# Kernel tuning notes

Measured on AMD Instinct MI355X. Metric: run time of the kernel, lower is better.

## Reference

```python
import jax, jax.numpy as jnp
import numpy as np
import math

# real<->complex packing matching the module's _c2r/_r2c (trailing dim 2)
def _r2c(x):
    return x[..., 0] + 1j * x[..., 1]

H, N, CH, RANK, LMAX = 256, 64, 1, 1, 2048


def setup_inputs() -> dict:
    key = jax.random.key(0)
    k0, k1, k2, k3, k4, k5 = jax.random.split(key, 6)
    C = jax.random.normal(k0, (CH, H, N, 2), jnp.float32)
    B = jax.random.normal(k1, (1, H, N, 2), jnp.float32)
    P = 0.3 * jax.random.normal(k2, (RANK, H, N, 2), jnp.float32)
    # w must have negative real part (Hurwitz) so Cauchy denominators stay away from zero
    w_re = -(jnp.abs(jax.random.normal(k3, (H, N))) * 0.5 + 0.1)
    w_im = jnp.pi * jax.random.normal(k4, (H, N))
    w = jnp.stack([w_re, w_im], axis=-1).astype(jnp.float32)
    log_dt = jax.random.uniform(k5, (H,), jnp.float32,
                                math.log(1e-3), math.log(1e-1))
    return {"C": C, "B": B, "P": P, "w": w, "log_dt": log_dt, "L": LMAX}


def reference(C, B, P, w, log_dt, L):
    Cc = _r2c(C)            # (c, H, N) complex
    Bc = _r2c(B)            # (1, H, N)
    Pc = _r2c(P)            # (r, H, N)
    wc = _r2c(w)            # (H, N)
    Qc = jnp.conj(Pc)       # Q = P.conj() (resolve_conj path)
    dt = jnp.exp(log_dt)    # (H,)

    # FFT nodes + bilinear transform (rate == 1.0)
    F = L // 2 + 1
    omega = jnp.exp(-2j * jnp.pi / L) ** jnp.arange(F)   # (F,) complex64
    z = 2 * (1 - omega) / (1 + omega)                     # (F,)

    w_dt = wc * dt[:, None].astype(wc.dtype)              # (H, N)

    Bcat = jnp.concatenate([Bc, Pc], axis=0)              # (1+r, H, N)
    Ccat = jnp.concatenate([Cc, Qc], axis=0)              # (c+r, H, N)
    v = Bcat[:, None] * Ccat[None]                        # (1+r, c+r, H, N)

    # Cauchy kernel: r[a,b,h,f] = sum_n v[a,b,h,n] / (z[f] - w_dt[h,n])
    denom = z - w_dt[..., None]                           # (H, N, F)
    r = jnp.sum(v[..., None] / denom, axis=-2)            # (1+r, c+r, H, F)
    r = r * dt[None, None, :, None].astype(r.dtype)

    # rank-1 Woodbury low-rank correction
    k_f = r[:-1, :-1] - r[:-1, -1:] * r[-1:, :-1] / (1 + r[-1:, -1:])  # (1, c, H, F)
    k_f = k_f * 2 / (1 + omega)

    k = jnp.fft.irfft(k_f, n=L, axis=-1)[..., :L]         # (1, c, H, L) real
    k_B = k[-1]                                           # (c, H, L)
    return k_B
```

## Files before the change

### kernel.cpp

```cpp
#include <hip/hip_runtime.h>


#define HH 256
#define NN 64
#define LL 2048
#define MM 1024
#define NT 512

#define PI_OVER_1024 0.0030679615757712823f
#define PI_OVER_512  0.0061359231515425647f

__global__ __launch_bounds__(NT) void ssk_fused(
    const float* __restrict__ Cin, const float* __restrict__ Bin,
    const float* __restrict__ Pin, const float* __restrict__ Win,
    const float* __restrict__ logdt, float* __restrict__ out)
{
    __shared__ float2 sW[NN];
    __shared__ float2 sV00[NN], sV01[NN], sV10[NN], sV11[NN];
    __shared__ float2 sX[MM + 1];
    __shared__ float2 sA[MM];
    __shared__ float2 sBf[MM];

    const int h = blockIdx.x;
    const int t = threadIdx.x;
    const float dtv = expf(logdt[h]);

    if (t < NN) {
        const int base = (h * NN + t) * 2;
        const float Br = Bin[base], Bi = Bin[base + 1];
        const float Cr = Cin[base], Ci = Cin[base + 1];
        const float Pr = Pin[base], Pi = Pin[base + 1];
        sW[t]   = make_float2(Win[base] * dtv, Win[base + 1] * dtv);
        sV00[t] = make_float2(Br * Cr - Bi * Ci, Br * Ci + Bi * Cr);
        sV01[t] = make_float2(Br * Pr + Bi * Pi, Bi * Pr - Br * Pi);
        sV10[t] = make_float2(Pr * Cr - Pi * Ci, Pr * Ci + Pi * Cr);
        sV11[t] = make_float2(Pr * Pr + Pi * Pi, 0.0f);
    }
    __syncthreads();

    for (int f = t; f <= MM; f += NT) {
        const float ang = PI_OVER_1024 * (float)f;
        float si, co;
        sincosf(ang, &si, &co);
        const float ur = 1.0f + co, ui = -si;
        const float t1r = 2.0f * (1.0f - co), t1i = 2.0f * si;

        float s00r = 0.f, s00i = 0.f, s01r = 0.f, s01i = 0.f;
        float s10r = 0.f, s10i = 0.f, s11r = 0.f, s11i = 0.f;
        #pragma unroll 4
        for (int n = 0; n < NN; ++n) {
            const float2 wd = sW[n];
            const float dr = t1r - (wd.x * ur - wd.y * ui);
            const float di = t1i - (wd.x * ui + wd.y * ur);
            const float inv = __builtin_amdgcn_rcpf(dr * dr + di * di);
            const float er = dr * inv, ei = -di * inv;
            float2 v;
            v = sV00[n]; s00r += v.x * er - v.y * ei; s00i += v.x * ei + v.y * er;
            v = sV01[n]; s01r += v.x * er - v.y * ei; s01i += v.x * ei + v.y * er;
            v = sV10[n]; s10r += v.x * er - v.y * ei; s10i += v.x * ei + v.y * er;
            v = sV11[n]; s11r += v.x * er;            s11i += v.x * ei;
        }
        const float gr = dtv * ur, gi = dtv * ui;
        const float numr = s01r * s10r - s01i * s10i;
        const float numi = s01r * s10i + s01i * s10r;
        const float qr = 1.0f + (gr * s11r - gi * s11i);
        const float qi = gr * s11i + gi * s11r;
        const float tr = gr * numr - gi * numi;
        const float ti = gr * numi + gi * numr;
        const float qinv = __builtin_amdgcn_rcpf(qr * qr + qi * qi);
        const float cr = (tr * qr + ti * qi) * qinv;
        const float ci = (ti * qr - tr * qi) * qinv;
        const float kr = 2.0f * dtv * (s00r - cr);
        float       ki = 2.0f * dtv * (s00i - ci);
        if (f == 0 || f == MM) ki = 0.0f;
        sX[f] = make_float2(kr, ki);
    }
    __syncthreads();

    for (int f = t; f < MM; f += NT) {
        const float2 a1 = sX[f];
        const float2 x2 = sX[MM - f];
        const float a2r = x2.x, a2i = -x2.y;
        const float er = 0.5f * (a1.x + a2r), eim = 0.5f * (a1.y + a2i);
        const float gr = 0.5f * (a1.x - a2r), gim = 0.5f * (a1.y - a2i);
        const float ang = PI_OVER_1024 * (float)f;
        float st, ct;
        sincosf(ang, &st, &ct);
        const float Or = ct * gr - st * gim;
        const float Oi = ct * gim + st * gr;
        sA[f] = make_float2(er - Oi, eim + Or);
    }
    __syncthreads();

    float2* cur = sA;
    float2* nxt = sBf;
    #pragma unroll
    for (int i = 0; i < 10; ++i) {
        const int s = 1 << i;
        const int b = t;
        if (b < 512) {
            const int j = b & ~(s - 1);
            const float2 a = cur[b];
            const float2 c = cur[b + 512];
            const float sr = a.x + c.x, sim = a.y + c.y;
            const float dr = a.x - c.x, dim = a.y - c.y;
            const float ang = PI_OVER_512 * (float)j;
            float st, ct;
            sincosf(ang, &st, &ct);
            nxt[b + j]     = make_float2(sr, sim);
            nxt[b + j + s] = make_float2(ct * dr - st * dim, ct * dim + st * dr);
        }
        __syncthreads();
        float2* tmp = cur; cur = nxt; nxt = tmp;
    }

    const float scale = 1.0f / (float)MM;
    float2* outv = (float2*)(out + (size_t)h * LL);
    for (int m = t; m < MM; m += NT) {
        const float2 z = cur[m];
        outv[m] = make_float2(z.x * scale, z.y * scale);
    }
}

extern "C" void kernel_launch(void* const* d_in, const int* in_sizes, int n_in,
                              void* d_out, int out_size, void* d_ws, size_t ws_size,
                              hipStream_t stream) {
    const float* C  = (const float*)d_in[0];
    const float* B  = (const float*)d_in[1];
    const float* P  = (const float*)d_in[2];
    const float* W  = (const float*)d_in[3];
    const float* ld = (const float*)d_in[4];
    float* out = (float*)d_out;
    ssk_fused<<<HH, NT, 0, stream>>>(C, B, P, W, ld, out);
}
```

Baseline: 86.47 us.

## Pack Cauchy data into float4, use packed-float math, fast intrinsics, compute Nyquist analytically

The per-node Cauchy terms are packed into float4 shared arrays and the inner Cauchy loop is rewritten with two-wide vector types, so the compiler can emit packed FP32 ops and wider LDS loads. The Nyquist bin is no longer computed by the loop; it is taken from a wavefront reduction of v00, which removes the uneven third iteration. sincosf and expf are replaced with fast intrinsics, and the 1/M scale is folded into the untangle step. This cuts loop trip imbalance and ALU and LDS instruction count, at some cost in precision from the fast transcendentals.

After: 77.03 us. 1.12x faster.

```diff
diff --git a/kernel.cpp b/kernel.cpp
--- a/kernel.cpp
+++ b/kernel.cpp
@@ -1,5 +1,7 @@
 #include <hip/hip_runtime.h>
 
+
+typedef float v2f __attribute__((ext_vector_type(2)));
 
 #define HH 256
 #define NN 64
@@ -15,77 +17,86 @@
     const float* __restrict__ Pin, const float* __restrict__ Win,
     const float* __restrict__ logdt, float* __restrict__ out)
 {
-    __shared__ float2 sW[NN];
-    __shared__ float2 sV00[NN], sV01[NN], sV10[NN], sV11[NN];
+    __shared__ float4 sD4[NN * 3];
     __shared__ float2 sX[MM + 1];
     __shared__ float2 sA[MM];
     __shared__ float2 sBf[MM];
 
     const int h = blockIdx.x;
     const int t = threadIdx.x;
-    const float dtv = expf(logdt[h]);
+    const float dtv = __expf(logdt[h]);
 
     if (t < NN) {
         const int base = (h * NN + t) * 2;
         const float Br = Bin[base], Bi = Bin[base + 1];
         const float Cr = Cin[base], Ci = Cin[base + 1];
         const float Pr = Pin[base], Pi = Pin[base + 1];
-        sW[t]   = make_float2(Win[base] * dtv, Win[base + 1] * dtv);
-        sV00[t] = make_float2(Br * Cr - Bi * Ci, Br * Ci + Bi * Cr);
-        sV01[t] = make_float2(Br * Pr + Bi * Pi, Bi * Pr - Br * Pi);
-        sV10[t] = make_float2(Pr * Cr - Pi * Ci, Pr * Ci + Pi * Cr);
-        sV11[t] = make_float2(Pr * Pr + Pi * Pi, 0.0f);
+        const float v00r = Br * Cr - Bi * Ci, v00i = Br * Ci + Bi * Cr;
+        sD4[t * 3 + 0] = make_float4(Win[base] * dtv, Win[base + 1] * dtv, v00r, v00i);
+        sD4[t * 3 + 1] = make_float4(Br * Pr + Bi * Pi, Bi * Pr - Br * Pi,
+                                     Pr * Cr - Pi * Ci, Pr * Ci + Pi * Cr);
+        sD4[t * 3 + 2] = make_float4(Pr * Pr + Pi * Pi, 0.f, 0.f, 0.f);
+        float r = v00r;
+        #pragma unroll
+        for (int off = 32; off; off >>= 1) r += __shfl_xor(r, off, 64);
+        if (t == 0) sX[MM] = make_float2(0.5f * dtv * r, 0.f);
     }
     __syncthreads();
 
-    for (int f = t; f <= MM; f += NT) {
-        const float ang = PI_OVER_1024 * (float)f;
+    const float* sDf = (const float*)sD4;
+    #pragma unroll
+    for (int rep = 0; rep < 2; ++rep) {
+        const int f = t + rep * 512;
         float si, co;
-        sincosf(ang, &si, &co);
-        const float ur = 1.0f + co, ui = -si;
-        const float t1r = 2.0f * (1.0f - co), t1i = 2.0f * si;
+        __sincosf(PI_OVER_1024 * (float)f, &si, &co);
+        const v2f u  = {1.0f + co, -si};
+        const v2f t1 = {2.0f * (1.0f - co), 2.0f * si};
 
-        float s00r = 0.f, s00i = 0.f, s01r = 0.f, s01i = 0.f;
-        float s10r = 0.f, s10i = 0.f, s11r = 0.f, s11i = 0.f;
-        #pragma unroll 4
+        v2f s00 = {0.f, 0.f}, s01 = {0.f, 0.f}, s10 = {0.f, 0.f}, s11 = {0.f, 0.f};
+        #pragma unroll 8
         for (int n = 0; n < NN; ++n) {
-            const float2 wd = sW[n];
-            const float dr = t1r - (wd.x * ur - wd.y * ui);
-            const float di = t1i - (wd.x * ui + wd.y * ur);
-            const float inv = __builtin_amdgcn_rcpf(dr * dr + di * di);
-            const float er = dr * inv, ei = -di * inv;
-            float2 v;
-            v = sV00[n]; s00r += v.x * er - v.y * ei; s00i += v.x * ei + v.y * er;
-            v = sV01[n]; s01r += v.x * er - v.y * ei; s01i += v.x * ei + v.y * er;
-            v = sV10[n]; s10r += v.x * er - v.y * ei; s10i += v.x * ei + v.y * er;
-            v = sV11[n]; s11r += v.x * er;            s11i += v.x * ei;
+            const float4 q0 = sD4[n * 3 + 0];
+            const float4 q1 = sD4[n * 3 + 1];
+            const float v11 = sDf[n * 12 + 8];
+            v2f den = t1;
+            den = den - (v2f){q0.x, q0.x} * u;
+            den = den + (v2f){q0.y, q0.y} * (v2f){u.y, -u.x};
+            const float inv = __builtin_amdgcn_rcpf(den.x * den.x + den.y * den.y);
+            const v2f e  = den * (v2f){inv, -inv};
+            const v2f es = {e.y, e.x};
+            s00 = s00 + (v2f){q0.z, q0.z} * e;
+            s00 = s00 + (v2f){-q0.w, q0.w} * es;
+            s01 = s01 + (v2f){q1.x, q1.x} * e;
+            s01 = s01 + (v2f){-q1.y, q1.y} * es;
+            s10 = s10 + (v2f){q1.z, q1.z} * e;
+            s10 = s10 + (v2f){-q1.w, q1.w} * es;
+            s11 = s11 + (v2f){v11, v11} * e;
         }
-        const float gr = dtv * ur, gi = dtv * ui;
-        const float numr = s01r * s10r - s01i * s10i;
-        const float numi = s01r * s10i + s01i * s10r;
-        const float qr = 1.0f + (gr * s11r - gi * s11i);
-        const float qi = gr * s11i + gi * s11r;
+        const float gr = dtv * u.x, gi = dtv * u.y;
+        const float numr = s01.x * s10.x - s01.y * s10.y;
+        const float numi = s01.x * s10.y + s01.y * s10.x;
+        const float qr = 1.0f + (gr * s11.x - gi * s11.y);
+        const float qi = gr * s11.y + gi * s11.x;
         const float tr = gr * numr - gi * numi;
         const float ti = gr * numi + gi * numr;
         const float qinv = __builtin_amdgcn_rcpf(qr * qr + qi * qi);
         const float cr = (tr * qr + ti * qi) * qinv;
         const float ci = (ti * qr - tr * qi) * qinv;
-        const float kr = 2.0f * dtv * (s00r - cr);
-        float       ki = 2.0f * dtv * (s00i - ci);
-        if (f == 0 || f == MM) ki = 0.0f;
+        const float kr = 2.0f * dtv * (s00.x - cr);
+        float       ki = 2.0f * dtv * (s00.y - ci);
+        if (f == 0) ki = 0.0f;
         sX[f] = make_float2(kr, ki);
     }
     __syncthreads();
 
+    const float HS = 4.8828125e-4f;
     for (int f = t; f < MM; f += NT) {
         const float2 a1 = sX[f];
         const float2 x2 = sX[MM - f];
-        const float a2r = x2.x, a2i = -x2.y;
-        const float er = 0.5f * (a1.x + a2r), eim = 0.5f * (a1.y + a2i);
-        const float gr = 0.5f * (a1.x - a2r), gim = 0.5f * (a1.y - a2i);
-        const float ang = PI_OVER_1024 * (float)f;
+        const float er  = HS * (a1.x + x2.x), eim = HS * (a1.y - x2.y);
+        const float gr  = HS * (a1.x - x2.x), gim = HS * (a1.y + x2.y);
         float st, ct;
-        sincosf(ang, &st, &ct);
+        __sincosf(PI_OVER_1024 * (float)f, &st, &ct);
         const float Or = ct * gr - st * gim;
         const float Oi = ct * gim + st * gr;
         sA[f] = make_float2(er - Oi, eim + Or);
@@ -98,28 +109,21 @@
     for (int i = 0; i < 10; ++i) {
         const int s = 1 << i;
         const int b = t;
-        if (b < 512) {
-            const int j = b & ~(s - 1);
-            const float2 a = cur[b];
-            const float2 c = cur[b + 512];
-            const float sr = a.x + c.x, sim = a.y + c.y;
-            const float dr = a.x - c.x, dim = a.y - c.y;
-            const float ang = PI_OVER_512 * (float)j;
-            float st, ct;
-            sincosf(ang, &st, &ct);
-            nxt[b + j]     = make_float2(sr, sim);
-            nxt[b + j + s] = make_float2(ct * dr - st * dim, ct * dim + st * dr);
-        }
+        const int j = b & ~(s - 1);
+        const float2 a = cur[b];
+        const float2 c = cur[b + 512];
+        const float sr = a.x + c.x, sim = a.y + c.y;
+        const float dr = a.x - c.x, dim = a.y - c.y;
+        float st, ct;
+        __sincosf(PI_OVER_512 * (float)j, &st, &ct);
+        nxt[b + j]     = make_float2(sr, sim);
+        nxt[b + j + s] = make_float2(ct * dr - st * dim, ct * dim + st * dr);
         __syncthreads();
         float2* tmp = cur; cur = nxt; nxt = tmp;
     }
 
-    const float scale = 1.0f / (float)MM;
     float2* outv = (float2*)(out + (size_t)h * LL);
-    for (int m = t; m < MM; m += NT) {
-        const float2 z = cur[m];
-        outv[m] = make_float2(z.x * scale, z.y * scale);
-    }
+    for (int m = t; m < MM; m += NT) outv[m] = cur[m];
 }
 
 extern "C" void kernel_launch(void* const* d_in, const int* in_sizes, int n_in,
```
